# Kernel optimization log

Hardware: AMD Instinct MI355X
Metric: run time of the kernel (lower is better)

## Reference

```python
import jax, jax.numpy as jnp
import numpy as np

N_NODES, N_EDGES, D, N_MOVIE, N_GENRE, L_MAX = 50000, 400000, 128, 20400, 30, 680
HOPS, HEADS, C_HEAD, N_LAYERS, T_HEADS, FF = 3, 4, 32, 4, 4, 2048


def _leaky(x, s):
    return jnp.where(x >= 0, x, s * x)


def _layer_norm(x, g, b, eps=1e-5):
    m = x.mean(-1, keepdims=True)
    v = ((x - m) ** 2).mean(-1, keepdims=True)
    return (x - m) / jnp.sqrt(v + eps) * g + b


def _gat_conv(x, ei, W, a_src, a_dst, b):
    # PyG GATConv: add self-loops, per-head linear, edge-softmax over incoming edges.
    N = x.shape[0]
    loop = jnp.arange(N)
    src = jnp.concatenate([ei[0], loop])
    dst = jnp.concatenate([ei[1], loop])
    h = (x @ W.T).reshape(N, HEADS, C_HEAD)
    al_s = (h * a_src[None]).sum(-1)  # [N, H]
    al_d = (h * a_dst[None]).sum(-1)
    e = _leaky(al_s[src] + al_d[dst], 0.2)  # [E+N, H]
    m = jax.ops.segment_max(e, dst, num_segments=N)
    ee = jnp.exp(e - m[dst])
    den = jax.ops.segment_sum(ee, dst, num_segments=N)
    alpha = ee / den[dst]
    out = jax.ops.segment_sum(h[src] * alpha[:, :, None], dst, num_segments=N)
    return out.reshape(N, HEADS * C_HEAD) + b


def _mha(y, pad_mask, qkv_w, qkv_b, out_w, out_b):
    B, S, Dm = y.shape
    hd = Dm // T_HEADS
    qkv = y @ qkv_w.T + qkv_b
    q, k, v = jnp.split(qkv, 3, axis=-1)
    q = q.reshape(B, S, T_HEADS, hd).transpose(0, 2, 1, 3)
    k = k.reshape(B, S, T_HEADS, hd).transpose(0, 2, 1, 3)
    v = v.reshape(B, S, T_HEADS, hd).transpose(0, 2, 1, 3)
    scores = jnp.einsum('bhqd,bhkd->bhqk', q, k) / jnp.sqrt(jnp.float32(hd))
    scores = jnp.where(pad_mask[:, None, None, :], -1e9, scores)
    a = jax.nn.softmax(scores, axis=-1)
    o = jnp.einsum('bhqk,bhkd->bhqd', a, v).transpose(0, 2, 1, 3).reshape(B, S, Dm)
    return o @ out_w.T + out_b


def _forward(x, e0, e1, e2, movie_idx, genre, gat_W, gat_att_src, gat_att_dst, gat_bias,
             dec_W, dec_b, qkv_w, qkv_b, out_w, out_b, ln1_g, ln1_b, ln2_g, ln2_b,
             ffn_w1, ffn_b1, ffn_w2, ffn_b2, fus_w, fus_b):
    edges = [e0, e1, e2]
    acc = jnp.zeros_like(x)
    for kk in range(HOPS):  # multi-hop GAT with exp hop decay (dropout off: eval)
        h = _gat_conv(x, edges[kk], gat_W[kk], gat_att_src[kk], gat_att_dst[kk], gat_bias[kk])
        h = _leaky(h @ dec_W[kk].T + dec_b[kk], 0.01)
        acc = acc + float(np.exp(-0.1 * kk)) * h
    x = acc
    xm = x[movie_idx]  # x[genre_mask]
    # group movie nodes into padded per-genre sequences [N_GENRE, L_MAX, D]
    onehot = jax.nn.one_hot(genre, N_GENRE, dtype=jnp.int32)
    pos = jnp.cumsum(onehot, axis=0)[jnp.arange(genre.shape[0]), genre] - 1
    counts = jnp.sum(onehot, axis=0)
    all_genre = jnp.zeros((N_GENRE, L_MAX, x.shape[1]), x.dtype).at[genre, pos].set(xm)
    pad_mask = jnp.arange(L_MAX)[None, :] >= counts[:, None]  # True = padding
    y = all_genre
    for l in range(N_LAYERS):  # PyTorch post-LN TransformerEncoder, relu FFN, eval dropout
        a = _mha(y, pad_mask, qkv_w[l], qkv_b[l], out_w[l], out_b[l])
        y = _layer_norm(y + a, ln1_g[l], ln1_b[l])
        f = jax.nn.relu(y @ ffn_w1[l].T + ffn_b1[l]) @ ffn_w2[l].T + ffn_b2[l]
        y = _layer_norm(y + f, ln2_g[l], ln2_b[l])
    # genre_backward: mean-pool per genre, gather back per node
    valid = (~pad_mask).astype(x.dtype)
    pooled = (y * valid[..., None]).sum(1) / jnp.maximum(valid.sum(1), 1.0)[:, None]
    emb = pooled[genre]
    fused = _leaky(jnp.concatenate([xm, emb], axis=1) @ fus_w.T + fus_b, 0.01)
    return x.at[movie_idx].set(fused)


def setup_inputs() -> dict:
    key = jax.random.key(0)
    ks = jax.random.split(key, 24)
    s = 0.05
    nrm = lambda i, shp: jax.random.normal(ks[i], shp, jnp.float32) * s
    return {
        'x': jax.random.normal(ks[0], (N_NODES, D), jnp.float32),
        'edge_index_hop0': jax.random.randint(ks[1], (2, N_EDGES), 0, N_NODES),
        'edge_index_hop1': jax.random.randint(ks[2], (2, N_EDGES), 0, N_NODES),
        'edge_index_hop2': jax.random.randint(ks[3], (2, N_EDGES), 0, N_NODES),
        'movie_idx': jnp.arange(N_MOVIE),
        'genre': jnp.arange(N_MOVIE) % N_GENRE,
        'gat_W': nrm(4, (HOPS, D, D)),
        'gat_att_src': nrm(5, (HOPS, HEADS, C_HEAD)),
        'gat_att_dst': nrm(6, (HOPS, HEADS, C_HEAD)),
        'gat_bias': nrm(7, (HOPS, D)),
        'dec_W': nrm(8, (HOPS, D, D)),
        'dec_b': nrm(9, (HOPS, D)),
        'qkv_w': nrm(10, (N_LAYERS, 3 * D, D)),
        'qkv_b': nrm(11, (N_LAYERS, 3 * D)),
        'out_w': nrm(12, (N_LAYERS, D, D)),
        'out_b': nrm(13, (N_LAYERS, D)),
        'ln1_g': jnp.ones((N_LAYERS, D), jnp.float32),
        'ln1_b': jnp.zeros((N_LAYERS, D), jnp.float32),
        'ln2_g': jnp.ones((N_LAYERS, D), jnp.float32),
        'ln2_b': jnp.zeros((N_LAYERS, D), jnp.float32),
        'ffn_w1': nrm(14, (N_LAYERS, FF, D)),
        'ffn_b1': nrm(15, (N_LAYERS, FF)),
        'ffn_w2': nrm(16, (N_LAYERS, D, FF)),
        'ffn_b2': nrm(17, (N_LAYERS, D)),
        'fus_w': nrm(18, (D, 2 * D)),
        'fus_b': nrm(19, (D,)),
    }


def reference(x, edge_index_hop0, edge_index_hop1, edge_index_hop2, movie_idx, genre,
              gat_W, gat_att_src, gat_att_dst, gat_bias, dec_W, dec_b,
              qkv_w, qkv_b, out_w, out_b, ln1_g, ln1_b, ln2_g, ln2_b,
              ffn_w1, ffn_b1, ffn_w2, ffn_b2, fus_w, fus_b):
    return _forward(x, edge_index_hop0, edge_index_hop1, edge_index_hop2, movie_idx, genre,
                    gat_W, gat_att_src, gat_att_dst, gat_bias, dec_W, dec_b,
                    qkv_w, qkv_b, out_w, out_b, ln1_g, ln1_b, ln2_g, ln2_b,
                    ffn_w1, ffn_b1, ffn_w2, ffn_b2, fus_w, fus_b)
```

## Files before the change

kernel.cpp:

```cpp
#include <hip/hip_runtime.h>

#define N_NODES  50000
#define N_EDGES  400000
#define DIM      128
#define N_MOVIE  20400
#define N_GENRE  30
#define L_MAX    680
#define NROWS    (N_GENRE * L_MAX)
#define FF       2048
#define N_LAYERS 4

#define NBKT 98
#define NPB  512
#define ECAP 4608
#define SCAP 5120
#define EPGB (NBKT * ECAP)
#define SPGB (NBKT * SCAP)

typedef __attribute__((ext_vector_type(8))) short bf16x8;
typedef __attribute__((ext_vector_type(4))) float f32x4;

#define MFMA16 __builtin_amdgcn_mfma_f32_16x16x32_bf16

__device__ __forceinline__ float b2f(ushort u) {
    union { unsigned i; float f; } c; c.i = ((unsigned)u) << 16; return c.f;
}
__device__ __forceinline__ ushort f2b(float f) {
    union { float f; unsigned i; } c; c.f = f;
    unsigned u = c.i;
    u += 0x7FFFu + ((u >> 16) & 1u);
    return (ushort)(u >> 16);
}
__device__ __forceinline__ bf16x8 load8s(const ushort* p) {
    return *(const bf16x8*)p;
}
__device__ __forceinline__ void async16(const ushort* g, ushort* l) {
    __builtin_amdgcn_global_load_lds(
        (const __attribute__((address_space(1))) void*)g,
        (__attribute__((address_space(3))) void*)l, 16, 0, 0);
}

__device__ __forceinline__ void cvt8(const float* s, ushort* d, int i) {
    const float4* q = (const float4*)(s + (size_t)i * 8);
    float4 a = q[0], b = q[1];
    bf16x8 r;
    r[0] = (short)f2b(a.x); r[1] = (short)f2b(a.y);
    r[2] = (short)f2b(a.z); r[3] = (short)f2b(a.w);
    r[4] = (short)f2b(b.x); r[5] = (short)f2b(b.y);
    r[6] = (short)f2b(b.z); r[7] = (short)f2b(b.w);
    *(bf16x8*)(d + (size_t)i * 8) = r;
}

__global__ void cvt32(const float* __restrict__ s, ushort* __restrict__ d, int n8)
{
    int i = blockIdx.x * blockDim.x + threadIdx.x;
    if (i < n8) cvt8(s, d, i);
}

__global__ void cvt_w(const float* gatW, const float* decW, const float* qkvW,
                      const float* outW, const float* fw1, const float* fw2,
                      const float* fusW,
                      ushort* gatWb, ushort* decWb, ushort* qkvWb,
                      ushort* outWb, ushort* fw1b, ushort* fw2b, ushort* fusWb)
{
    const float* s; ushort* d; int n8;
    switch (blockIdx.y) {
        case 0: s = gatW; d = gatWb; n8 = 49152 / 8; break;
        case 1: s = decW; d = decWb; n8 = 49152 / 8; break;
        case 2: s = qkvW; d = qkvWb; n8 = 196608 / 8; break;
        case 3: s = outW; d = outWb; n8 = 65536 / 8; break;
        case 4: s = fw1;  d = fw1b;  n8 = 1048576 / 8; break;
        case 5: s = fw2;  d = fw2b;  n8 = 1048576 / 8; break;
        default: s = fusW; d = fusWb; n8 = 32768 / 8; break;
    }
    int i = blockIdx.x * 256 + threadIdx.x;
    if (i < n8) cvt8(s, d, i);
}

template<int BM, int ACT, int EPI, int OBF>
__global__ __launch_bounds__(256) void gemm_lds(
    const ushort* __restrict__ A, const ushort* __restrict__ W,
    const float* __restrict__ bias, void* __restrict__ Cv,
    int M, int N, int K, float scale)
{
    __shared__ ushort smem[BM * 32 + 128 * 32];
    ushort* As = smem;
    ushort* Ws = smem + BM * 32;
    const int tid  = threadIdx.x;
    const int wave = tid >> 6, lane = tid & 63;
    const int quad = lane >> 4, l16 = lane & 15;
    const int m0 = blockIdx.x * BM;
    const int n0 = blockIdx.y * 128;

    constexpr int MT = BM / 32;
    const int mbase = (wave & 1) * (BM / 2);
    const int nbase = (wave >> 1) * 64;

    const int srow = wave * 16 + (lane >> 2);
    const int skof = (lane & 3) * 8;

    f32x4 acc[MT][4] = {};
    for (int k0 = 0; k0 < K; k0 += 32) {
#pragma unroll
        for (int i = 0; i < BM / 64; i++) {
            int r = i * 64 + srow;
            int rg = min(m0 + r, M - 1);
            async16(A + (size_t)rg * K + k0 + skof, As + r * 32 + skof);
        }
#pragma unroll
        for (int i = 0; i < 2; i++) {
            int r = i * 64 + srow;
            async16(W + (size_t)(n0 + r) * K + k0 + skof, Ws + r * 32 + skof);
        }
        __syncthreads();

        bf16x8 a[MT], b[4];
#pragma unroll
        for (int mt = 0; mt < MT; mt++)
            a[mt] = load8s(As + (mbase + mt * 16 + l16) * 32 + quad * 8);
#pragma unroll
        for (int nt = 0; nt < 4; nt++)
            b[nt] = load8s(Ws + (nbase + nt * 16 + l16) * 32 + quad * 8);
#pragma unroll
        for (int mt = 0; mt < MT; mt++)
#pragma unroll
            for (int nt = 0; nt < 4; nt++)
                acc[mt][nt] = MFMA16(a[mt], b[nt], acc[mt][nt], 0, 0, 0);
        __syncthreads();
    }

    if constexpr (OBF == 1) {
        static_assert(BM == 128, "OBF=1 staged epilogue assumes BM=128");
        ushort* Cs = smem;
#pragma unroll
        for (int p = 0; p < 2; p++) {
            if ((wave & 1) == p) {
#pragma unroll
                for (int nt = 0; nt < 4; nt++) {
                    const int col = nbase + nt * 16 + l16;
                    const float bv = bias ? bias[n0 + col] : 0.f;
#pragma unroll
                    for (int mt = 0; mt < MT; mt++) {
                        const int rl = mt * 16 + quad * 4;
#pragma unroll
                        for (int r = 0; r < 4; r++) {
                            float v = acc[mt][nt][r] + bv;
                            if (ACT == 1) v = (v >= 0.f) ? v : 0.01f * v;
                            if (ACT == 2) v = fmaxf(v, 0.f);
                            Cs[(rl + r) * 128 + col] = f2b(v);
                        }
                    }
                }
            }
            __syncthreads();
            const int row = tid >> 2, cb = (tid & 3) * 32;
            const int grow = m0 + p * 64 + row;
            if (grow < M) {
                const ushort* s = Cs + row * 128 + cb;
                ushort* dp = (ushort*)Cv + (size_t)grow * N + n0 + cb;
                *(int4*)(dp)      = *(const int4*)(s);
                *(int4*)(dp + 8)  = *(const int4*)(s + 8);
                *(int4*)(dp + 16) = *(const int4*)(s + 16);
                *(int4*)(dp + 24) = *(const int4*)(s + 24);
            }
            __syncthreads();
        }
    } else {
#pragma unroll
        for (int nt = 0; nt < 4; nt++) {
            const int col = n0 + nbase + nt * 16 + l16;
            const float bv = bias ? bias[col] : 0.f;
#pragma unroll
            for (int mt = 0; mt < MT; mt++) {
                if (OBF == 2) {
                    const int row0 = m0 + mbase + mt * 16 + quad * 4;
                    if (row0 < M) {
                        ushort4 pk;
                        pk.x = f2b(acc[mt][nt][0] + bv);
                        pk.y = f2b(acc[mt][nt][1] + bv);
                        pk.z = f2b(acc[mt][nt][2] + bv);
                        pk.w = f2b(acc[mt][nt][3] + bv);
                        *(ushort4*)((ushort*)Cv + (size_t)col * M + row0) = pk;
                    }
                } else {
#pragma unroll
                    for (int r = 0; r < 4; r++) {
                        const int row = m0 + mbase + mt * 16 + quad * 4 + r;
                        if (row < M) {
                            float v = acc[mt][nt][r] + bv;
                            if (ACT == 1) v = (v >= 0.f) ? v : 0.01f * v;
                            if (ACT == 2) v = fmaxf(v, 0.f);
                            const size_t idx = (size_t)row * N + col;
                            if (EPI == 1) ((float*)Cv)[idx] += scale * v;
                            else          ((float*)Cv)[idx] = v;
                        }
                    }
                }
            }
        }
    }
}

__global__ __launch_bounds__(256, 2) void ffn_fused(
    const ushort* __restrict__ y, const ushort* __restrict__ w1,
    const float* __restrict__ b1, const ushort* __restrict__ w2,
    const float* __restrict__ b2,
    float* __restrict__ o0, float* __restrict__ o1,
    float* __restrict__ o2, float* __restrict__ o3, int M)
{
    __shared__ ushort f1s[2][32 * 128];
    __shared__ ushort f2s[2][128 * 32];
    __shared__ ushort mids[4][32 * 40];

    const int tid  = threadIdx.x;
    const int wave = tid >> 6, lane = tid & 63;
    const int quad = lane >> 4, l16 = lane & 15;
    const int m0 = blockIdx.x * 128;
    const int fh = blockIdx.y;
    const int fbase = fh * (FF / 4);
    float* o = (fh == 0) ? o0 : (fh == 1) ? o1 : (fh == 2) ? o2 : o3;

    const int sw1 = ((tid & 15) ^ (tid >> 4)) * 8;
    const int sw2 = ((tid & 3) ^ ((tid >> 3) & 3)) * 8;

    const int wrow = m0 + wave * 32;
    bf16x8 yf[2][4];
#pragma unroll
    for (int mt = 0; mt < 2; mt++) {
        const int mr = min(wrow + mt * 16 + l16, M - 1);
#pragma unroll
        for (int ks = 0; ks < 4; ks++)
            yf[mt][ks] = load8s(y + (size_t)mr * 128 + ks * 32 + quad * 8);
    }

#pragma unroll
    for (int i = 0; i < 2; i++) {
        int row = i * 16 + (tid >> 4);
        async16(w1 + (size_t)(fbase + row) * 128 + sw1,
                f1s[0] + row * 128 + (tid & 15) * 8);
    }
#pragma unroll
    for (int i = 0; i < 2; i++) {
        int row = i * 64 + (tid >> 2);
        async16(w2 + (size_t)row * FF + fbase + sw2,
                f2s[0] + row * 32 + (tid & 3) * 8);
    }

    f32x4 oacc[2][8] = {};
    ushort* midw = mids[wave];
    int cur = 0;
    __syncthreads();

    for (int fo = 0; fo < FF / 4; fo += 32) {
        if (fo + 32 < FF / 4) {
            const int fn = fbase + fo + 32;
#pragma unroll
            for (int i = 0; i < 2; i++) {
                int row = i * 16 + (tid >> 4);
                async16(w1 + (size_t)(fn + row) * 128 + sw1,
                        f1s[cur ^ 1] + row * 128 + (tid & 15) * 8);
            }
#pragma unroll
            for (int i = 0; i < 2; i++) {
                int row = i * 64 + (tid >> 2);
                async16(w2 + (size_t)row * FF + fn + sw2,
                        f2s[cur ^ 1] + row * 32 + (tid & 3) * 8);
            }
        }
        const ushort* F1 = f1s[cur];
        const ushort* F2 = f2s[cur];

        f32x4 midacc[2][2] = {};
#pragma unroll
        for (int ks = 0; ks < 4; ks++) {
            const int csA = (((ks * 4 + quad) ^ l16) & 15) * 8;
#pragma unroll
            for (int ft = 0; ft < 2; ft++) {
                bf16x8 wf = load8s(F1 + (ft * 16 + l16) * 128 + csA);
                midacc[0][ft] = MFMA16(wf, yf[0][ks], midacc[0][ft], 0, 0, 0);
                midacc[1][ft] = MFMA16(wf, yf[1][ks], midacc[1][ft], 0, 0, 0);
            }
        }
#pragma unroll
        for (int mt = 0; mt < 2; mt++)
#pragma unroll
            for (int ft = 0; ft < 2; ft++) {
                const float4 bb = *(const float4*)(b1 + fbase + fo + ft * 16 + quad * 4);
                ushort4 pk;
                pk.x = f2b(fmaxf(midacc[mt][ft][0] + bb.x, 0.f));
                pk.y = f2b(fmaxf(midacc[mt][ft][1] + bb.y, 0.f));
                pk.z = f2b(fmaxf(midacc[mt][ft][2] + bb.z, 0.f));
                pk.w = f2b(fmaxf(midacc[mt][ft][3] + bb.w, 0.f));
                *(ushort4*)(midw + (mt * 16 + l16) * 40 + ft * 16 + quad * 4) = pk;
            }
        bf16x8 mf0 = load8s(midw + (size_t)l16 * 40 + quad * 8);
        bf16x8 mf1 = load8s(midw + (size_t)(16 + l16) * 40 + quad * 8);
        const int gB = (quad ^ ((l16 >> 1) & 3)) * 8;
#pragma unroll
        for (int dt = 0; dt < 8; dt++) {
            bf16x8 wf = load8s(F2 + (dt * 16 + l16) * 32 + gB);
            oacc[0][dt] = MFMA16(wf, mf0, oacc[0][dt], 0, 0, 0);
            oacc[1][dt] = MFMA16(wf, mf1, oacc[1][dt], 0, 0, 0);
        }
        __syncthreads();
        cur ^= 1;
    }

#pragma unroll
    for (int mt = 0; mt < 2; mt++) {
        const int m = wrow + mt * 16 + l16;
        if (m < M) {
            float* op = o + (size_t)m * 128 + quad * 4;
#pragma unroll
            for (int dt = 0; dt < 8; dt++) {
                float4 v;
                if (fh == 0) {
                    const float4 bv = *(const float4*)(b2 + dt * 16 + quad * 4);
                    v.x = oacc[mt][dt][0] + bv.x;
                    v.y = oacc[mt][dt][1] + bv.y;
                    v.z = oacc[mt][dt][2] + bv.z;
                    v.w = oacc[mt][dt][3] + bv.w;
                } else {
                    v.x = oacc[mt][dt][0];
                    v.y = oacc[mt][dt][1];
                    v.z = oacc[mt][dt][2];
                    v.w = oacc[mt][dt][3];
                }
                *(float4*)(op + dt * 16) = v;
            }
        }
    }
}

__global__ void gat_al(const ushort* __restrict__ h,
                       const float* __restrict__ asrc, const float* __restrict__ adst,
                       float* __restrict__ als, float* __restrict__ ald, int N)
{
    int idx = blockIdx.x * blockDim.x + threadIdx.x;
    if (idx >= N * 4) return;
    int n = idx >> 2, hh = idx & 3;
    const ushort* hp = h + (size_t)n * DIM + hh * 32;
    float s = 0.f, d = 0.f;
#pragma unroll
    for (int q = 0; q < 4; q++) {
        bf16x8 hv = load8s(hp + q * 8);
#pragma unroll
        for (int c = 0; c < 8; c++) {
            float v = b2f((ushort)hv[c]);
            s += v * asrc[hh * 32 + q * 8 + c];
            d += v * adst[hh * 32 + q * 8 + c];
        }
    }
    als[idx] = s; ald[idx] = d;
}

__global__ void csr_initb(int* __restrict__ bcur)
{
    int i = blockIdx.x * 256 + threadIdx.x;
    if (i < 3 * NBKT) bcur[i * 16] = (i % NBKT) * ECAP;
}

__global__ __launch_bounds__(256) void csr_route(
    const int* __restrict__ e0, const int* __restrict__ e1, const int* __restrict__ e2,
    int* __restrict__ bcur, int* __restrict__ ebuf)
{
    __shared__ int hist[NBKT], base[NBKT], cur[NBKT];
    const int g = blockIdx.y, t = threadIdx.x;
    const int* e = (g == 0) ? e0 : (g == 1) ? e1 : e2;
    const int i0 = blockIdx.x * 4096;
    for (int j = t; j < NBKT; j += 256) { hist[j] = 0; cur[j] = 0; }
    __syncthreads();
    unsigned pk[16]; int bk[16];
#pragma unroll
    for (int j = 0; j < 16; j++) {
        int i = i0 + j * 256 + t;
        if (i < N_EDGES) {
            int s = e[i], d = e[N_EDGES + i];
            bk[j] = d >> 9;
            pk[j] = (unsigned)s | ((unsigned)(d & 511) << 16);
            atomicAdd(&hist[bk[j]], 1);
        } else bk[j] = -1;
    }
    __syncthreads();
    for (int j = t; j < NBKT; j += 256)
        if (hist[j]) base[j] = atomicAdd(&bcur[(g * NBKT + j) * 16], hist[j]);
    __syncthreads();
#pragma unroll
    for (int j = 0; j < 16; j++)
        if (bk[j] >= 0) {
            int p = base[bk[j]] + atomicAdd(&cur[bk[j]], 1);
            ebuf[(size_t)g * EPGB + p] = (int)pk[j];
        }
}

__global__ __launch_bounds__(256) void csr_build(
    const int* __restrict__ bcur, const int* __restrict__ ebuf,
    int* __restrict__ off, int* __restrict__ deg, int* __restrict__ srcs)
{
    __shared__ int hist[NPB];
    __shared__ int part[256];
    const int g = blockIdx.y, b = blockIdx.x, t = threadIdx.x;
    const int nb0 = b * NPB;
    const int nn = min(NPB, N_NODES - nb0);
    const int cnt = bcur[(g * NBKT + b) * 16] - b * ECAP;
    const int* eb = ebuf + (size_t)g * EPGB + b * ECAP;

    for (int j = t; j < NPB; j += 256) hist[j] = (j < nn) ? 1 : 0;
    __syncthreads();
    for (int i = t; i < cnt; i += 256)
        atomicAdd(&hist[(eb[i] >> 16) & 511], 1);
    __syncthreads();

    int a0 = hist[t * 2], a1 = hist[t * 2 + 1];
    int sum = a0 + a1;
    part[t] = sum;
    __syncthreads();
    for (int d = 1; d < 256; d <<= 1) {
        int x = (t >= d) ? part[t - d] : 0;
        __syncthreads();
        part[t] += x;
        __syncthreads();
    }
    const int excl = part[t] - sum;
    __syncthreads();
    const int sb = b * SCAP;
    hist[t * 2]     = excl;
    hist[t * 2 + 1] = excl + a0;
    if (t * 2 < nn) {
        off[(size_t)g * N_NODES + nb0 + t * 2] = sb + excl;
        deg[(size_t)g * N_NODES + nb0 + t * 2] = a0;
    }
    if (t * 2 + 1 < nn) {
        off[(size_t)g * N_NODES + nb0 + t * 2 + 1] = sb + excl + a0;
        deg[(size_t)g * N_NODES + nb0 + t * 2 + 1] = a1;
    }
    __syncthreads();

    int* sg = srcs + (size_t)g * SPGB + sb;
    for (int i = t; i < cnt; i += 256) {
        int v = eb[i];
        int p = atomicAdd(&hist[(v >> 16) & 511], 1);
        sg[p] = v & 0xFFFF;
    }
    for (int j = t; j < nn; j += 256) {
        int p = atomicAdd(&hist[j], 1);
        sg[p] = nb0 + j;
    }
}

__global__ __launch_bounds__(256) void gat_gather(
    const int* __restrict__ off, const int* __restrict__ deg, const int* __restrict__ srcs,
    const ushort* __restrict__ hb, const float* __restrict__ als,
    const float* __restrict__ ald, const float* __restrict__ bias,
    ushort* __restrict__ ob)
{
    int w = (blockIdx.x * 256 + threadIdx.x) >> 6;
    int lane = threadIdx.x & 63;
    if (w >= N_NODES) return;
    const int grp  = lane >> 4;
    const int l16  = lane & 15;
    const int head = l16 >> 2;
    const float adv = ald[(size_t)w * 4 + head];
    const int jb = off[w], dg = deg[w];

    float acc[8] = {};
    float wsum = 0.f;

    int j = grp;
    int s = (j < dg) ? srcs[jb + j] : 0;
    while (j < dg) {
        const int jn = j + 4;
        const int sn = (jn < dg) ? srcs[jb + jn] : 0;
        bf16x8 hv = load8s(hb + (size_t)s * DIM + l16 * 8);
        float e = als[(size_t)s * 4 + head] + adv;
        e = (e >= 0.f) ? e : 0.2f * e;
        const float wg = __expf(e);
        wsum += wg;
#pragma unroll
        for (int c = 0; c < 8; c++) acc[c] += wg * b2f((ushort)hv[c]);
        j = jn; s = sn;
    }

    wsum += __shfl_xor(wsum, 16, 64);
    wsum += __shfl_xor(wsum, 32, 64);
#pragma unroll
    for (int c = 0; c < 8; c++) {
        acc[c] += __shfl_xor(acc[c], 16, 64);
        acc[c] += __shfl_xor(acc[c], 32, 64);
    }

    if (grp == 0) {
        const float inv = 1.f / wsum;
        bf16x8 r;
#pragma unroll
        for (int c = 0; c < 8; c++)
            r[c] = (short)f2b(acc[c] * inv + bias[l16 * 8 + c]);
        *(bf16x8*)(ob + (size_t)w * DIM + l16 * 8) = r;
    }
}

__global__ void calc_pos(const int* __restrict__ genre, int* __restrict__ pos,
                         int* __restrict__ cnt, int NM)
{
    int i = blockIdx.x * blockDim.x + threadIdx.x;
    if (i < NM) pos[i] = atomicAdd(&cnt[genre[i]], 1);
}

__global__ void build_y(const float* __restrict__ acc, const int* __restrict__ midx,
                        const int* __restrict__ genre, const int* __restrict__ pos,
                        float* __restrict__ y, ushort* __restrict__ yb)
{
    int i = blockIdx.x, c = threadIdx.x;
    int g = genre[i], p = pos[i];
    float v = acc[(size_t)midx[i] * DIM + c];
    size_t o = ((size_t)g * L_MAX + p) * DIM + c;
    y[o] = v; yb[o] = f2b(v);
}

#define SP 40

__global__ __launch_bounds__(256) void flash_attn(
    const ushort* __restrict__ qk, const ushort* __restrict__ vtg,
    const int* __restrict__ cnt, ushort* __restrict__ o)
{
    __shared__ ushort Pb[4][32 * SP];

    const int qt = blockIdx.x, hh = blockIdx.y, g = blockIdx.z;
    const int t = threadIdx.x, wave = t >> 6, lane = t & 63;
    const int quad = lane >> 4, l16 = lane & 15;
    const int L = cnt[g];
    const float scale = 0.17677669529663687f;
    const ushort* base = qk + (size_t)g * L_MAX * 256;
    const ushort* vb0 = vtg + (size_t)(hh * 32 + l16) * NROWS + g * L_MAX;
    const ushort* vb1 = vb0 + (size_t)16 * NROWS;

    const int q0 = qt * 128 + wave * 32;
    bf16x8 a0 = load8s(base + (size_t)min(q0 + l16,      L_MAX - 1) * 256 + hh * 32 + quad * 8);
    bf16x8 a1 = load8s(base + (size_t)min(q0 + 16 + l16, L_MAX - 1) * 256 + hh * 32 + quad * 8);

    f32x4 oacc[2][2] = {};
    float rsum[2] = {0.f, 0.f};
    ushort* P = Pb[wave];

    for (int kt = 0; kt < 704; kt += 32) {
        bf16x8 b0 = load8s(base + (size_t)min(kt + l16,      L_MAX - 1) * 256 + 128 + hh * 32 + quad * 8);
        bf16x8 b1 = load8s(base + (size_t)min(kt + 16 + l16, L_MAX - 1) * 256 + 128 + hh * 32 + quad * 8);
        f32x4 z = {};
        f32x4 st00 = MFMA16(b0, a0, z, 0, 0, 0);
        f32x4 st01 = MFMA16(b0, a1, z, 0, 0, 0);
        f32x4 st10 = MFMA16(b1, a0, z, 0, 0, 0);
        f32x4 st11 = MFMA16(b1, a1, z, 0, 0, 0);

        const int kc0 = kt + quad * 4, kc1 = kt + 16 + quad * 4;
#pragma unroll
        for (int qh = 0; qh < 2; qh++) {
            const f32x4 sA = qh ? st01 : st00;
            const f32x4 sB = qh ? st11 : st10;
            float w[8];
#pragma unroll
            for (int r = 0; r < 4; r++) {
                w[r]     = (kc0 + r < L) ? __expf(sA[r] * scale) : 0.f;
                w[4 + r] = (kc1 + r < L) ? __expf(sB[r] * scale) : 0.f;
                rsum[qh] += w[r] + w[4 + r];
            }
            ushort4 pk0, pk1;
            pk0.x = f2b(w[0]); pk0.y = f2b(w[1]); pk0.z = f2b(w[2]); pk0.w = f2b(w[3]);
            pk1.x = f2b(w[4]); pk1.y = f2b(w[5]); pk1.z = f2b(w[6]); pk1.w = f2b(w[7]);
            *(ushort4*)(P + (qh * 16 + l16) * SP + quad * 4)      = pk0;
            *(ushort4*)(P + (qh * 16 + l16) * SP + 16 + quad * 4) = pk1;
        }
        bf16x8 p0 = load8s(P + (size_t)l16 * SP + quad * 8);
        bf16x8 p1 = load8s(P + (size_t)(16 + l16) * SP + quad * 8);
        bf16x8 v0 = load8s(vb0 + kt + quad * 8);
        bf16x8 v1 = load8s(vb1 + kt + quad * 8);
        oacc[0][0] = MFMA16(v0, p0, oacc[0][0], 0, 0, 0);
        oacc[0][1] = MFMA16(v0, p1, oacc[0][1], 0, 0, 0);
        oacc[1][0] = MFMA16(v1, p0, oacc[1][0], 0, 0, 0);
        oacc[1][1] = MFMA16(v1, p1, oacc[1][1], 0, 0, 0);
    }

#pragma unroll
    for (int qh = 0; qh < 2; qh++) {
        float s = rsum[qh];
        s += __shfl_xor(s, 16, 64);
        s += __shfl_xor(s, 32, 64);
        const int q = q0 + qh * 16 + l16;
        if (q < L_MAX) {
            const float inv = 1.f / s;
#pragma unroll
            for (int dh = 0; dh < 2; dh++) {
                ushort4 pk;
                pk.x = f2b(oacc[dh][qh][0] * inv);
                pk.y = f2b(oacc[dh][qh][1] * inv);
                pk.z = f2b(oacc[dh][qh][2] * inv);
                pk.w = f2b(oacc[dh][qh][3] * inv);
                *(ushort4*)(o + ((size_t)(g * L_MAX + q)) * DIM + hh * 32 + dh * 16 + quad * 4) = pk;
            }
        }
    }
}

__global__ __launch_bounds__(128) void ln_res(
    float* __restrict__ y, const float* __restrict__ res,
    const float* __restrict__ res2, const float* __restrict__ res3,
    const float* __restrict__ res4,
    const float* __restrict__ g, const float* __restrict__ b,
    ushort* __restrict__ yb)
{
    __shared__ float sh[2], sh2[2];
    const int r = blockIdx.x, t = threadIdx.x;
    const size_t base = (size_t)r * DIM;
    float v = y[base + t] + res[base + t];
    if (res2) v += res2[base + t];
    if (res3) v += res3[base + t] + res4[base + t];
    float s = v;
    for (int off = 32; off; off >>= 1) s += __shfl_down(s, off, 64);
    if ((t & 63) == 0) sh[t >> 6] = s;
    __syncthreads();
    const float mean = (sh[0] + sh[1]) * (1.f / 128.f);
    const float d = v - mean;
    float q = d * d;
    for (int off = 32; off; off >>= 1) q += __shfl_down(q, off, 64);
    if ((t & 63) == 0) sh2[t >> 6] = q;
    __syncthreads();
    const float var = (sh2[0] + sh2[1]) * (1.f / 128.f);
    float o = d * rsqrtf(var + 1e-5f) * g[t] + b[t];
    y[base + t] = o; yb[base + t] = f2b(o);
}

__global__ __launch_bounds__(256) void pool_partial(
    const float* __restrict__ y, const int* __restrict__ cnt, float* __restrict__ pooled)
{
    __shared__ float sh[128];
    const int g = blockIdx.x, seg = blockIdx.y, t = threadIdx.x;
    const int c = t & 127, h = t >> 7;
    const int L = cnt[g];
    const int k0 = seg * 40, k1 = min(k0 + 40, L);
    float s = 0.f;
    for (int k = k0 + h; k < k1; k += 2) s += y[((size_t)g * L_MAX + k) * DIM + c];
    if (h) sh[c] = s;
    __syncthreads();
    if (!h) {
        float tot = s + sh[c];
        if (k0 < L) atomicAdd(&pooled[g * DIM + c], tot / (float)max(L, 1));
    }
}

__global__ void build_fin(const float* __restrict__ acc, const float* __restrict__ pooled,
                          const int* __restrict__ midx, const int* __restrict__ genre,
                          ushort* __restrict__ A2)
{
    const int i = blockIdx.x, t = threadIdx.x;
    float v = (t < 128) ? acc[(size_t)midx[i] * DIM + t]
                        : pooled[genre[i] * DIM + (t - 128)];
    A2[(size_t)i * 256 + t] = f2b(v);
}

__global__ void scatter_movies(const float* __restrict__ fused, const int* __restrict__ midx,
                               float* __restrict__ out)
{
    const int i = blockIdx.x, c = threadIdx.x;
    out[(size_t)midx[i] * DIM + c] = fused[(size_t)i * DIM + c];
}

extern "C" void kernel_launch(void* const* d_in, const int* in_sizes, int n_in,
                              void* d_out, int out_size, void* d_ws, size_t ws_size,
                              hipStream_t stream)
{
    const float* x      = (const float*)d_in[0];
    const int* e[3]     = { (const int*)d_in[1], (const int*)d_in[2], (const int*)d_in[3] };
    const int* midx     = (const int*)d_in[4];
    const int* genre    = (const int*)d_in[5];
    const float* gatW   = (const float*)d_in[6];
    const float* attS   = (const float*)d_in[7];
    const float* attD   = (const float*)d_in[8];
    const float* gatB   = (const float*)d_in[9];
    const float* decW   = (const float*)d_in[10];
    const float* decB   = (const float*)d_in[11];
    const float* qkvW   = (const float*)d_in[12];
    const float* qkvB   = (const float*)d_in[13];
    const float* outW   = (const float*)d_in[14];
    const float* outB   = (const float*)d_in[15];
    const float* ln1g   = (const float*)d_in[16];
    const float* ln1b   = (const float*)d_in[17];
    const float* ln2g   = (const float*)d_in[18];
    const float* ln2b   = (const float*)d_in[19];
    const float* fw1    = (const float*)d_in[20];
    const float* fb1    = (const float*)d_in[21];
    const float* fw2    = (const float*)d_in[22];
    const float* fb2    = (const float*)d_in[23];
    const float* fusW   = (const float*)d_in[24];
    const float* fusB   = (const float*)d_in[25];
    float* out = (float*)d_out;

    float* ws  = (float*)d_ws;
    float* acc = ws;
    float* R   = ws + 6400000;
    ushort* xb   = (ushort*)(R);
    ushort* hb   = (ushort*)(R + 3200000);
    ushort* gbx  = (ushort*)(R + 6400000);
    float*  als  = R + 9600000;
    float*  ald  = R + 9800000;
    int*   bcur  = (int*)(R + 10000000);
    int*   ebuf  = (int*)(R + 10004736);
    int*   off3  = (int*)(R + 11359488);
    int*   deg3  = (int*)(R + 11509488);
    int*   srcs3 = (int*)(R + 11659488);
    ushort* gatWb= (ushort*)(R + 13164768);
    ushort* decWb= (ushort*)(R + 13189344);
    float*  ybuf  = R;
    float*  tmp   = R + 2611200;
    ushort* ybx   = (ushort*)(R + 5222400);
    ushort* attnb = (ushort*)(R + 6528000);
    ushort* qkvb  = (ushort*)(R + 7833600);
    ushort* vtg   = (ushort*)(R + 10444800);
    ushort* finb  = (ushort*)(R + 11750400);
    float*  tmp2  = R + 14361600;
    float*  tmp3  = R + 16972800;
    float*  tmp4  = R + 19584000;
    float*  pooled= R + 22195200;
    int*    cntb  = (int*)(R + 22199040);
    int*    posb  = cntb + 32;
    ushort* qkvWb = (ushort*)(R + 22220000);
    ushort* outWb = (ushort*)(R + 22318304);
    ushort* fw1b  = (ushort*)(R + 22351072);
    ushort* fw2b  = (ushort*)(R + 22875360);
    ushort* fusWb = (ushort*)(R + 23399648);

    const float decay[3] = { 1.0f, 0.90483741803595952f, 0.81873075307798182f };

    cvt_w<<<dim3(512, 7), 256, 0, stream>>>(
        gatW, decW, qkvW, outW, fw1, fw2, fusW,
        gatWb, decWb, qkvWb, outWb, fw1b, fw2b, fusWb);
    cvt32<<<(6400000 / 8 + 255) / 256, 256, 0, stream>>>(x, xb, 6400000 / 8);

    csr_initb<<<(3 * NBKT + 255) / 256, 256, 0, stream>>>(bcur);
    csr_route<<<dim3((N_EDGES + 4095) / 4096, 3), 256, 0, stream>>>(
        e[0], e[1], e[2], bcur, ebuf);
    csr_build<<<dim3(NBKT, 3), 256, 0, stream>>>(bcur, ebuf, off3, deg3, srcs3);

    for (int k = 0; k < 3; k++) {
        gemm_lds<128, 0, 0, 1><<<dim3(391, 1), 256, 0, stream>>>(
            xb, gatWb + k * DIM * DIM, nullptr, hb, N_NODES, DIM, DIM, 1.f);
        gat_al<<<(N_NODES * 4 + 255) / 256, 256, 0, stream>>>(
            hb, attS + k * DIM, attD + k * DIM, als, ald, N_NODES);
        gat_gather<<<(N_NODES * 64 + 255) / 256, 256, 0, stream>>>(
            off3 + (size_t)k * N_NODES, deg3 + (size_t)k * N_NODES,
            srcs3 + (size_t)k * SPGB, hb, als, ald, gatB + k * DIM, gbx);
        if (k == 0)
            gemm_lds<128, 1, 0, 0><<<dim3(391, 1), 256, 0, stream>>>(
                gbx, decWb, decB, acc, N_NODES, DIM, DIM, 1.f);
        else
            gemm_lds<128, 1, 1, 0><<<dim3(391, 1), 256, 0, stream>>>(
                gbx, decWb + k * DIM * DIM, decB + k * DIM, acc, N_NODES, DIM, DIM, decay[k]);
    }

    hipMemsetAsync(cntb, 0, 32 * 4, stream);
    calc_pos<<<(N_MOVIE + 255) / 256, 256, 0, stream>>>(genre, posb, cntb, N_MOVIE);
    build_y<<<N_MOVIE, 128, 0, stream>>>(acc, midx, genre, posb, ybuf, ybx);

    for (int l = 0; l < N_LAYERS; l++) {
        gemm_lds<128, 0, 0, 1><<<dim3(160, 2), 256, 0, stream>>>(
            ybx, qkvWb + (size_t)l * 384 * DIM, qkvB + l * 384, qkvb, NROWS, 256, DIM, 1.f);
        gemm_lds<128, 0, 0, 2><<<dim3(160, 1), 256, 0, stream>>>(
            ybx, qkvWb + (size_t)l * 384 * DIM + 256 * DIM, qkvB + l * 384 + 256,
            vtg, NROWS, DIM, DIM, 1.f);
        flash_attn<<<dim3(6, 4, 30), 256, 0, stream>>>(qkvb, vtg, cntb, attnb);
        gemm_lds<64, 0, 0, 0><<<dim3(319, 1), 256, 0, stream>>>(
            attnb, outWb + (size_t)l * DIM * DIM, outB + l * DIM, tmp, NROWS, DIM, DIM, 1.f);
        ln_res<<<NROWS, 128, 0, stream>>>(ybuf, tmp, nullptr, nullptr, nullptr,
                                          ln1g + l * DIM, ln1b + l * DIM, ybx);
        ffn_fused<<<dim3((NROWS + 127) / 128, 4), 256, 0, stream>>>(
            ybx, fw1b + (size_t)l * FF * DIM, fb1 + (size_t)l * FF,
            fw2b + (size_t)l * DIM * FF, fb2 + (size_t)l * DIM,
            tmp, tmp2, tmp3, tmp4, NROWS);
        ln_res<<<NROWS, 128, 0, stream>>>(ybuf, tmp, tmp2, tmp3, tmp4,
                                          ln2g + l * DIM, ln2b + l * DIM, ybx);
    }

    hipMemsetAsync(pooled, 0, 3840 * 4, stream);
    pool_partial<<<dim3(N_GENRE, 17), 256, 0, stream>>>(ybuf, cntb, pooled);
    build_fin<<<N_MOVIE, 256, 0, stream>>>(acc, pooled, midx, genre, finb);
    gemm_lds<64, 1, 0, 0><<<dim3(319, 1), 256, 0, stream>>>(
        finb, fusWb, fusB, tmp, NROWS, DIM, 256, 1.f);

    hipMemcpyAsync(out, acc, (size_t)6400000 * 4, hipMemcpyDeviceToDevice, stream);
    scatter_movies<<<N_MOVIE, 128, 0, stream>>>(tmp, midx, out);
}
```

Baseline: 938.1 us.

## Load FFN weights directly from global memory and use wave-per-row LayerNorm

The fused FFN kernel drops its double-buffered LDS staging of W1 and W2 tiles and the per-iteration barriers. Each lane now reads its MFMA weight fragments straight from global memory and relies on L1/L2 caching, since all blocks share the same weights. Separately, the residual LayerNorm kernel now handles one row per wavefront with float2 loads and xor-shuffle reductions, four rows per block, and no shared memory or __syncthreads. The risk is that the direct weight loads are strided and uncoalesced and no longer prefetched ahead of use, which could stall the MFMA pipeline.

Measured after the change: 1.190 ms. +26.8%, slower.

```diff
diff --git a/kernel.cpp b/kernel.cpp
--- a/kernel.cpp
+++ b/kernel.cpp
@@ -208,8 +208,6 @@
     float* __restrict__ o0, float* __restrict__ o1,
     float* __restrict__ o2, float* __restrict__ o3, int M)
 {
-    __shared__ ushort f1s[2][32 * 128];
-    __shared__ ushort f2s[2][128 * 32];
     __shared__ ushort mids[4][32 * 40];
 
     const int tid  = threadIdx.x;
@@ -220,9 +218,6 @@
     const int fbase = fh * (FF / 4);
     float* o = (fh == 0) ? o0 : (fh == 1) ? o1 : (fh == 2) ? o2 : o3;
 
-    const int sw1 = ((tid & 15) ^ (tid >> 4)) * 8;
-    const int sw2 = ((tid & 3) ^ ((tid >> 3) & 3)) * 8;
-
     const int wrow = m0 + wave * 32;
     bf16x8 yf[2][4];
 #pragma unroll
@@ -233,50 +228,20 @@
             yf[mt][ks] = load8s(y + (size_t)mr * 128 + ks * 32 + quad * 8);
     }
 
-#pragma unroll
-    for (int i = 0; i < 2; i++) {
-        int row = i * 16 + (tid >> 4);
-        async16(w1 + (size_t)(fbase + row) * 128 + sw1,
-                f1s[0] + row * 128 + (tid & 15) * 8);
-    }
-#pragma unroll
-    for (int i = 0; i < 2; i++) {
-        int row = i * 64 + (tid >> 2);
-        async16(w2 + (size_t)row * FF + fbase + sw2,
-                f2s[0] + row * 32 + (tid & 3) * 8);
-    }
+    const ushort* w1l = w1 + (size_t)(fbase + l16) * 128 + quad * 8;
+    const ushort* w2l = w2 + (size_t)l16 * FF + fbase + quad * 8;
 
     f32x4 oacc[2][8] = {};
     ushort* midw = mids[wave];
-    int cur = 0;
-    __syncthreads();
 
     for (int fo = 0; fo < FF / 4; fo += 32) {
-        if (fo + 32 < FF / 4) {
-            const int fn = fbase + fo + 32;
-#pragma unroll
-            for (int i = 0; i < 2; i++) {
-                int row = i * 16 + (tid >> 4);
-                async16(w1 + (size_t)(fn + row) * 128 + sw1,
-                        f1s[cur ^ 1] + row * 128 + (tid & 15) * 8);
-            }
-#pragma unroll
-            for (int i = 0; i < 2; i++) {
-                int row = i * 64 + (tid >> 2);
-                async16(w2 + (size_t)row * FF + fn + sw2,
-                        f2s[cur ^ 1] + row * 32 + (tid & 3) * 8);
-            }
-        }
-        const ushort* F1 = f1s[cur];
-        const ushort* F2 = f2s[cur];
-
         f32x4 midacc[2][2] = {};
 #pragma unroll
-        for (int ks = 0; ks < 4; ks++) {
-            const int csA = (((ks * 4 + quad) ^ l16) & 15) * 8;
-#pragma unroll
-            for (int ft = 0; ft < 2; ft++) {
-                bf16x8 wf = load8s(F1 + (ft * 16 + l16) * 128 + csA);
+        for (int ft = 0; ft < 2; ft++) {
+            const ushort* wr = w1l + (size_t)(fo + ft * 16) * 128;
+#pragma unroll
+            for (int ks = 0; ks < 4; ks++) {
+                bf16x8 wf = load8s(wr + ks * 32);
                 midacc[0][ft] = MFMA16(wf, yf[0][ks], midacc[0][ft], 0, 0, 0);
                 midacc[1][ft] = MFMA16(wf, yf[1][ks], midacc[1][ft], 0, 0, 0);
             }
@@ -295,15 +260,12 @@
             }
         bf16x8 mf0 = load8s(midw + (size_t)l16 * 40 + quad * 8);
         bf16x8 mf1 = load8s(midw + (size_t)(16 + l16) * 40 + quad * 8);
-        const int gB = (quad ^ ((l16 >> 1) & 3)) * 8;
 #pragma unroll
         for (int dt = 0; dt < 8; dt++) {
-            bf16x8 wf = load8s(F2 + (dt * 16 + l16) * 32 + gB);
+            bf16x8 wf = load8s(w2l + (size_t)dt * 16 * FF + fo);
             oacc[0][dt] = MFMA16(wf, mf0, oacc[0][dt], 0, 0, 0);
             oacc[1][dt] = MFMA16(wf, mf1, oacc[1][dt], 0, 0, 0);
         }
-        __syncthreads();
-        cur ^= 1;
     }
 
 #pragma unroll
@@ -600,32 +562,49 @@
     }
 }
 
-__global__ __launch_bounds__(128) void ln_res(
+__global__ __launch_bounds__(256) void ln_res(
     float* __restrict__ y, const float* __restrict__ res,
     const float* __restrict__ res2, const float* __restrict__ res3,
     const float* __restrict__ res4,
     const float* __restrict__ g, const float* __restrict__ b,
     ushort* __restrict__ yb)
 {
-    __shared__ float sh[2], sh2[2];
-    const int r = blockIdx.x, t = threadIdx.x;
-    const size_t base = (size_t)r * DIM;
-    float v = y[base + t] + res[base + t];
-    if (res2) v += res2[base + t];
-    if (res3) v += res3[base + t] + res4[base + t];
-    float s = v;
-    for (int off = 32; off; off >>= 1) s += __shfl_down(s, off, 64);
-    if ((t & 63) == 0) sh[t >> 6] = s;
-    __syncthreads();
-    const float mean = (sh[0] + sh[1]) * (1.f / 128.f);
-    const float d = v - mean;
-    float q = d * d;
-    for (int off = 32; off; off >>= 1) q += __shfl_down(q, off, 64);
-    if ((t & 63) == 0) sh2[t >> 6] = q;
-    __syncthreads();
-    const float var = (sh2[0] + sh2[1]) * (1.f / 128.f);
-    float o = d * rsqrtf(var + 1e-5f) * g[t] + b[t];
-    y[base + t] = o; yb[base + t] = f2b(o);
+    const int r = blockIdx.x * 4 + (threadIdx.x >> 6);
+    const int lane = threadIdx.x & 63;
+    const size_t base = (size_t)r * DIM + lane * 2;
+    float2 v = *(const float2*)(y + base);
+    {
+        float2 a = *(const float2*)(res + base);
+        v.x += a.x; v.y += a.y;
+    }
+    if (res2) {
+        float2 a = *(const float2*)(res2 + base);
+        v.x += a.x; v.y += a.y;
+    }
+    if (res3) {
+        float2 a = *(const float2*)(res3 + base);
+        float2 c = *(const float2*)(res4 + base);
+        v.x += a.x + c.x; v.y += a.y + c.y;
+    }
+    float s = v.x + v.y;
+#pragma unroll
+    for (int off = 32; off; off >>= 1) s += __shfl_xor(s, off, 64);
+    const float mean = s * (1.f / 128.f);
+    const float dx = v.x - mean, dy = v.y - mean;
+    float q = dx * dx + dy * dy;
+#pragma unroll
+    for (int off = 32; off; off >>= 1) q += __shfl_xor(q, off, 64);
+    const float rst = rsqrtf(q * (1.f / 128.f) + 1e-5f);
+    const float2 gg = *(const float2*)(g + lane * 2);
+    const float2 bb = *(const float2*)(b + lane * 2);
+    float2 ov;
+    ov.x = dx * rst * gg.x + bb.x;
+    ov.y = dy * rst * gg.y + bb.y;
+    *(float2*)(y + base) = ov;
+    ushort2 pk;
+    pk.x = f2b(ov.x);
+    pk.y = f2b(ov.y);
+    *(ushort2*)(yb + base) = pk;
 }
 
 __global__ __launch_bounds__(256) void pool_partial(
@@ -768,14 +747,14 @@
         flash_attn<<<dim3(6, 4, 30), 256, 0, stream>>>(qkvb, vtg, cntb, attnb);
         gemm_lds<64, 0, 0, 0><<<dim3(319, 1), 256, 0, stream>>>(
             attnb, outWb + (size_t)l * DIM * DIM, outB + l * DIM, tmp, NROWS, DIM, DIM, 1.f);
-        ln_res<<<NROWS, 128, 0, stream>>>(ybuf, tmp, nullptr, nullptr, nullptr,
-                                          ln1g + l * DIM, ln1b + l * DIM, ybx);
+        ln_res<<<NROWS / 4, 256, 0, stream>>>(ybuf, tmp, nullptr, nullptr, nullptr,
+                                              ln1g + l * DIM, ln1b + l * DIM, ybx);
         ffn_fused<<<dim3((NROWS + 127) / 128, 4), 256, 0, stream>>>(
             ybx, fw1b + (size_t)l * FF * DIM, fb1 + (size_t)l * FF,
             fw2b + (size_t)l * DIM * FF, fb2 + (size_t)l * DIM,
             tmp, tmp2, tmp3, tmp4, NROWS);
-        ln_res<<<NROWS, 128, 0, stream>>>(ybuf, tmp, tmp2, tmp3, tmp4,
-                                          ln2g + l * DIM, ln2b + l * DIM, ybx);
+        ln_res<<<NROWS / 4, 256, 0, stream>>>(ybuf, tmp, tmp2, tmp3, tmp4,
+                                              ln2g + l * DIM, ln2b + l * DIM, ybx);
     }
 
     hipMemsetAsync(pooled, 0, 3840 * 4, stream);
```
